# Optimization experiments

Measured on AMD Instinct MI355X. Metric: run time of the kernel, lower is better.

Reference implementation:

```python
import jax, jax.numpy as jnp
import numpy as np

N = 6144
F_IN, H1, H2, EMB = 512, 256, 128, 64
ALPHA = 0.2  # LeakyReLU negative slope
NEG_INF = -9e15


def setup_inputs() -> dict:
    key = jax.random.key(0)
    ks = jax.random.split(key, 12)
    x = jax.random.normal(ks[0], (N, F_IN), dtype=jnp.float32)
    adj = (jax.random.uniform(ks[1], (N, N)) < 0.01).astype(jnp.float32)
    adj = jnp.maximum(adj, jnp.eye(N, dtype=jnp.float32))
    M = jax.random.uniform(ks[2], (N, N), dtype=jnp.float32)

    def glorot(k, shape):
        lim = float(np.sqrt(6.0 / (shape[0] + shape[1])))
        return jax.random.uniform(k, shape, jnp.float32, -lim, lim)

    params = {
        "W1": glorot(ks[3], (F_IN, H1)), "a_s1": glorot(ks[4], (H1, 1)), "a_n1": glorot(ks[5], (H1, 1)),
        "W2": glorot(ks[6], (H1, H2)),  "a_s2": glorot(ks[7], (H2, 1)), "a_n2": glorot(ks[8], (H2, 1)),
        "W3": glorot(ks[9], (H2, EMB)), "a_s3": glorot(ks[10], (EMB, 1)), "a_n3": glorot(ks[11], (EMB, 1)),
    }
    return {"x": x, "adj": adj, "M": M, **params}


def _gat_layer(x, adj, M, W, a_s, a_n):
    h = x @ W                                   # [N, d_out]
    e = (h @ a_s) + (h @ a_n).T                 # [N, N] pairwise logits
    e = jax.nn.leaky_relu(e * M, ALPHA)
    e = jnp.where(adj > 0, e, NEG_INF)
    att = jax.nn.softmax(e, axis=1)             # masked row softmax
    return jax.nn.elu(att @ h)


def reference(x, adj, M, W1, a_s1, a_n1, W2, a_s2, a_n2, W3, a_s3, a_n3):
    h = _gat_layer(x, adj, M, W1, a_s1, a_n1)
    h = _gat_layer(h, adj, M, W2, a_s2, a_n2)
    h = _gat_layer(h, adj, M, W3, a_s3, a_n3)
    z = h / jnp.maximum(jnp.linalg.norm(h, axis=1, keepdims=True), 1e-12)
    A_pred = jax.nn.sigmoid(z @ z.T)
    return (A_pred, z)
```

## Files before the change

### kernel.cpp

```cpp
#include <hip/hip_runtime.h>
#include <hip/hip_bf16.h>
#include <math.h>

#define NROW 6144
#define LRELU_ALPHA 0.2f
#define MAXD 128

typedef __attribute__((ext_vector_type(8))) __bf16 bf16x8;
typedef __attribute__((ext_vector_type(16))) float f32x16;

__global__ __launch_bounds__(256) void prep_small(
    const float* __restrict__ W1, const float* __restrict__ W2, const float* __restrict__ W3,
    __bf16* __restrict__ w1h, __bf16* __restrict__ w1l,
    __bf16* __restrict__ w2h, __bf16* __restrict__ w2l,
    __bf16* __restrict__ w3h, __bf16* __restrict__ w3l,
    const float* __restrict__ as1, const float* __restrict__ an1,
    const float* __restrict__ as2, const float* __restrict__ an2,
    const float* __restrict__ as3, const float* __restrict__ an3,
    float* __restrict__ wsa1, float* __restrict__ wna1,
    float* __restrict__ wsa2, float* __restrict__ wna2,
    float* __restrict__ wsa3, float* __restrict__ wna3) {
  int b = blockIdx.x;
  if (b < 672) {
    int idx = b * 256 + threadIdx.x;
    const float* W; __bf16 *wh, *wl; int K, D;
    if (idx < 131072) { W = W1; wh = w1h; wl = w1l; K = 512; D = 256; }
    else if (idx < 163840) { idx -= 131072; W = W2; wh = w2h; wl = w2l; K = 256; D = 128; }
    else { idx -= 163840; if (idx >= 8192) return; W = W3; wh = w3h; wl = w3l; K = 128; D = 64; }
    int k = idx / D, d = idx - k * D;
    float v = W[idx];
    __bf16 h = (__bf16)v;
    wh[(size_t)d * K + k] = h;
    wl[(size_t)d * K + k] = (__bf16)(v - (float)h);
    return;
  }
  int t = (b - 672) * 256 + threadIdx.x;
  if (t < 512) {
    float s = 0.f, n = 0.f;
    for (int d = 0; d < 256; ++d) { float w = W1[t * 256 + d]; s = fmaf(w, as1[d], s); n = fmaf(w, an1[d], n); }
    wsa1[t] = s; wna1[t] = n;
  } else if (t < 768) {
    int k = t - 512;
    float s = 0.f, n = 0.f;
    for (int d = 0; d < 128; ++d) { float w = W2[k * 128 + d]; s = fmaf(w, as2[d], s); n = fmaf(w, an2[d], n); }
    wsa2[k] = s; wna2[k] = n;
  } else if (t < 896) {
    int k = t - 768;
    float s = 0.f, n = 0.f;
    for (int d = 0; d < 64; ++d) { float w = W3[k * 64 + d]; s = fmaf(w, as3[d], s); n = fmaf(w, an3[d], n); }
    wsa3[k] = s; wna3[k] = n;
  }
}

__global__ __launch_bounds__(256) void build_csr(const float* __restrict__ adj,
                                                 const float* __restrict__ Mm,
                                                 int* __restrict__ cnt,
                                                 int* __restrict__ cidx,
                                                 float* __restrict__ cmval) {
  const int row = blockIdx.x;
  const int wv = threadIdx.x >> 6, lane = threadIdx.x & 63;
  __shared__ int wtot[4];
  __shared__ int jsh[MAXD];
  const float4* arow = (const float4*)(adj + (size_t)row * NROW);
  uint32_t mask = 0;
#pragma unroll
  for (int it = 0; it < 6; ++it) {
    float4 a = arow[wv * 384 + it * 64 + lane];
    uint32_t q = (a.x > 0.f ? 1u : 0u) | (a.y > 0.f ? 2u : 0u) |
                 (a.z > 0.f ? 4u : 0u) | (a.w > 0.f ? 8u : 0u);
    mask |= q << (it * 4);
  }
  const int pc = __popc(mask);
  int pre = pc;
#pragma unroll
  for (int off = 1; off < 64; off <<= 1) {
    int t = __shfl_up(pre, off);
    if (lane >= off) pre += t;
  }
  if (lane == 63) wtot[wv] = pre;
  __syncthreads();
  int base = pre - pc;
  for (int w = 0; w < wv; ++w) base += wtot[w];
  const int total = min(wtot[0] + wtot[1] + wtot[2] + wtot[3], MAXD);
  uint32_t m = mask;
  int p = base;
  const int cbase = wv * 1536 + lane * 4;
  while (m) {
    int b = __ffs(m) - 1;
    m &= m - 1;
    if (p < MAXD) jsh[p] = cbase + ((b >> 2) << 8) + (b & 3);
    ++p;
  }
  __syncthreads();
  const float* mrow = Mm + (size_t)row * NROW;
  for (int k = threadIdx.x; k < total; k += 256) {
    int j = jsh[k];
    cidx[(size_t)row * MAXD + k] = j;
    cmval[(size_t)row * MAXD + k] = mrow[j];
  }
  if (threadIdx.x == 0) cnt[row] = total;
}

__global__ __launch_bounds__(256) void gemm_mfma(const float* __restrict__ A,
                                                 const __bf16* __restrict__ Bth,
                                                 const __bf16* __restrict__ Btl,
                                                 const float* __restrict__ wsa,
                                                 const float* __restrict__ wna,
                                                 float* __restrict__ sv,
                                                 float* __restrict__ nv,
                                                 float* __restrict__ C,
                                                 __bf16* __restrict__ Cb, int K, int D) {
  const int wv = threadIdx.x >> 6, lane = threadIdx.x & 63;
  const int l31 = lane & 31, lh = lane >> 5;
  const int ib = blockIdx.x * 64 + (wv >> 1) * 32;
  const int jb = blockIdx.y * 64 + (wv & 1) * 32;
  const float* Arow = A + (size_t)(ib + l31) * K + lh * 8;
  const __bf16* Bh = Bth + (size_t)(jb + l31) * K + lh * 8;
  const __bf16* Bl = Btl + (size_t)(jb + l31) * K + lh * 8;
  const bool do_sn = (blockIdx.y == 0) && ((wv & 1) == 0);
  f32x16 acc;
#pragma unroll
  for (int r = 0; r < 16; ++r) acc[r] = 0.f;
  float ss = 0.f, nn = 0.f;
  for (int k = 0; k < K; k += 16) {
    float4 a0 = *(const float4*)(Arow + k);
    float4 a1 = *(const float4*)(Arow + k + 4);
    bf16x8 bh = *(const bf16x8*)(Bh + k);
    bf16x8 bl = *(const bf16x8*)(Bl + k);
    float av[8] = {a0.x, a0.y, a0.z, a0.w, a1.x, a1.y, a1.z, a1.w};
    if (do_sn) {
      float4 s0 = *(const float4*)(wsa + k + lh * 8);
      float4 s1 = *(const float4*)(wsa + k + lh * 8 + 4);
      float4 n0 = *(const float4*)(wna + k + lh * 8);
      float4 n1 = *(const float4*)(wna + k + lh * 8 + 4);
      ss = fmaf(av[0], s0.x, ss); ss = fmaf(av[1], s0.y, ss);
      ss = fmaf(av[2], s0.z, ss); ss = fmaf(av[3], s0.w, ss);
      ss = fmaf(av[4], s1.x, ss); ss = fmaf(av[5], s1.y, ss);
      ss = fmaf(av[6], s1.z, ss); ss = fmaf(av[7], s1.w, ss);
      nn = fmaf(av[0], n0.x, nn); nn = fmaf(av[1], n0.y, nn);
      nn = fmaf(av[2], n0.z, nn); nn = fmaf(av[3], n0.w, nn);
      nn = fmaf(av[4], n1.x, nn); nn = fmaf(av[5], n1.y, nn);
      nn = fmaf(av[6], n1.z, nn); nn = fmaf(av[7], n1.w, nn);
    }
    bf16x8 ah, al;
#pragma unroll
    for (int t = 0; t < 8; ++t) {
      __bf16 h = (__bf16)av[t];
      ah[t] = h;
      al[t] = (__bf16)(av[t] - (float)h);
    }
    acc = __builtin_amdgcn_mfma_f32_32x32x16_bf16(ah, bh, acc, 0, 0, 0);
    acc = __builtin_amdgcn_mfma_f32_32x32x16_bf16(ah, bl, acc, 0, 0, 0);
    acc = __builtin_amdgcn_mfma_f32_32x32x16_bf16(al, bh, acc, 0, 0, 0);
  }
  if (do_sn) {
    ss += __shfl_xor(ss, 32);
    nn += __shfl_xor(nn, 32);
    if (lh == 0) { sv[ib + l31] = ss; nv[ib + l31] = nn; }
  }
#pragma unroll
  for (int r = 0; r < 16; ++r) {
    int rowi = (r & 3) + 8 * (r >> 2) + 4 * lh;
    if (C)  C[(size_t)(ib + rowi) * D + jb + l31] = acc[r];
    if (Cb) Cb[(size_t)(ib + rowi) * D + jb + l31] = (__bf16)acc[r];
  }
}

template <int D, int WPR, bool BF16G, bool NORM>
__global__ __launch_bounds__(256) void attn_csr(const float* __restrict__ h,
                                                const __bf16* __restrict__ hb,
                                                const int* __restrict__ cnt,
                                                const int* __restrict__ cidx,
                                                const float* __restrict__ cmval,
                                                const float* __restrict__ sv,
                                                const float* __restrict__ nv,
                                                float* __restrict__ out,
                                                __bf16* __restrict__ zb) {
  constexpr int RPB = 4 / WPR;
  constexpr int CW = D / WPR;
  constexpr int NQ = BF16G ? 2 : CW / 64;
  __shared__ float ws[4][MAXD];
  __shared__ int js[4][MAXD];
  const int wv = threadIdx.x >> 6, lane = threadIdx.x & 63;
  const int row = blockIdx.x * RPB + wv / WPR;
  const int half = wv % WPR;
  const int c = cnt[row];
  const float si = sv[row];
  const size_t cb = (size_t)row * MAXD;

  float e0 = -1e30f, e1 = -1e30f;
  int j0 = 0, j1 = 0;
  if (lane < c) {
    j0 = cidx[cb + lane];
    float v = (si + nv[j0]) * cmval[cb + lane];
    e0 = v > 0.f ? v : LRELU_ALPHA * v;
  }
  if (lane + 64 < c) {
    j1 = cidx[cb + lane + 64];
    float v = (si + nv[j1]) * cmval[cb + lane + 64];
    e1 = v > 0.f ? v : LRELU_ALPHA * v;
  }
  float mx = fmaxf(e0, e1);
#pragma unroll
  for (int off = 32; off; off >>= 1) mx = fmaxf(mx, __shfl_xor(mx, off));
  float w0 = lane < c ? __expf(e0 - mx) : 0.f;
  float w1 = lane + 64 < c ? __expf(e1 - mx) : 0.f;
  float s = w0 + w1;
#pragma unroll
  for (int off = 32; off; off >>= 1) s += __shfl_xor(s, off);
  const float inv = 1.f / s;
  ws[wv][lane] = w0 * inv;
  ws[wv][lane + 64] = w1 * inv;
  js[wv][lane] = j0;
  js[wv][lane + 64] = j1;
  const int cbase = half * CW;
  float acc[NQ];
#pragma unroll
  for (int q = 0; q < NQ; ++q) acc[q] = 0.f;
  if (BF16G) {
#pragma unroll 8
    for (int k = 0; k < c; ++k) {
      const float wk = ws[wv][k];
      const uint32_t* hr = (const uint32_t*)(hb + (size_t)js[wv][k] * D + cbase);
      uint32_t v = hr[lane];
      acc[0] = fmaf(wk, __uint_as_float(v << 16), acc[0]);
      acc[1] = fmaf(wk, __uint_as_float(v & 0xffff0000u), acc[1]);
    }
    float2 o;
    o.x = acc[0] > 0.f ? acc[0] : expm1f(acc[0]);
    o.y = acc[1] > 0.f ? acc[1] : expm1f(acc[1]);
    *(float2*)(out + (size_t)row * D + cbase + lane * 2) = o;
  } else {
#pragma unroll 8
    for (int k = 0; k < c; ++k) {
      const float wk = ws[wv][k];
      const float* hr = h + (size_t)js[wv][k] * D + cbase;
#pragma unroll
      for (int q = 0; q < NQ; ++q) acc[q] = fmaf(wk, hr[lane + q * 64], acc[q]);
    }
    if (!NORM) {
#pragma unroll
      for (int q = 0; q < NQ; ++q) {
        float a = acc[q];
        out[(size_t)row * D + cbase + lane + q * 64] = a > 0.f ? a : expm1f(a);
      }
    } else {
      float a = acc[0];
      a = a > 0.f ? a : expm1f(a);
      float sq = a * a;
#pragma unroll
      for (int off = 32; off; off >>= 1) sq += __shfl_xor(sq, off);
      float zv = a / fmaxf(sqrtf(sq), 1e-12f);
      out[(size_t)row * 64 + lane] = zv;
      zb[(size_t)row * 64 + lane] = (__bf16)zv;
    }
  }
}

__global__ __launch_bounds__(256) void decoder_mfma(const __bf16* __restrict__ zb,
                                                    float* __restrict__ out) {
  const int wv = threadIdx.x >> 6, lane = threadIdx.x & 63;
  const int ib = blockIdx.y * 64 + (wv >> 1) * 32;
  const int jb = blockIdx.x * 64 + (wv & 1) * 32;
  const int l31 = lane & 31, lh = lane >> 5;
  const __bf16* Arow = zb + (size_t)(ib + l31) * 64 + lh * 8;
  const __bf16* Brow = zb + (size_t)(jb + l31) * 64 + lh * 8;
  f32x16 acc;
#pragma unroll
  for (int r = 0; r < 16; ++r) acc[r] = 0.f;
#pragma unroll
  for (int kk = 0; kk < 4; ++kk) {
    bf16x8 af = *(const bf16x8*)(Arow + kk * 16);
    bf16x8 bfv = *(const bf16x8*)(Brow + kk * 16);
    acc = __builtin_amdgcn_mfma_f32_32x32x16_bf16(af, bfv, acc, 0, 0, 0);
  }
#pragma unroll
  for (int r = 0; r < 16; ++r) {
    int rowi = (r & 3) + 8 * (r >> 2) + 4 * lh;
    float v = 1.f / (1.f + __expf(-acc[r]));
    out[(size_t)(ib + rowi) * NROW + jb + l31] = v;
  }
}

extern "C" void kernel_launch(void* const* d_in, const int* in_sizes, int n_in,
                              void* d_out, int out_size, void* d_ws, size_t ws_size,
                              hipStream_t stream) {
  const float* x   = (const float*)d_in[0];
  const float* adj = (const float*)d_in[1];
  const float* Mm  = (const float*)d_in[2];
  const float* W1  = (const float*)d_in[3];
  const float* as1 = (const float*)d_in[4];
  const float* an1 = (const float*)d_in[5];
  const float* W2  = (const float*)d_in[6];
  const float* as2 = (const float*)d_in[7];
  const float* an2 = (const float*)d_in[8];
  const float* W3  = (const float*)d_in[9];
  const float* as3 = (const float*)d_in[10];
  const float* an3 = (const float*)d_in[11];

  float* out = (float*)d_out;
  float* z = out + (size_t)NROW * NROW;

  float* ws = (float*)d_ws;
  float* hA   = ws;
  float* hB   = hA + (size_t)NROW * 256;
  float* sv   = hB + (size_t)NROW * 256;
  float* nv   = sv + NROW;
  float* cmv  = nv + NROW;
  int*   cix  = (int*)(cmv + (size_t)NROW * MAXD);
  int*   cct  = cix + (size_t)NROW * MAXD;
  __bf16* zb  = (__bf16*)(cct + NROW);
  __bf16* w1h = zb + (size_t)NROW * 64;
  __bf16* w1l = w1h + 512 * 256;
  __bf16* w2h = w1l + 512 * 256;
  __bf16* w2l = w2h + 256 * 128;
  __bf16* w3h = w2l + 256 * 128;
  __bf16* w3l = w3h + 128 * 64;
  float* wsa1 = (float*)(w3l + 128 * 64);
  float* wna1 = wsa1 + 512;
  float* wsa2 = wna1 + 512;
  float* wna2 = wsa2 + 256;
  float* wsa3 = wna2 + 256;
  float* wna3 = wsa3 + 128;
  __bf16* hAb = (__bf16*)(wna3 + 128);

  dim3 b256(256);

  prep_small<<<dim3(676), b256, 0, stream>>>(
      W1, W2, W3, w1h, w1l, w2h, w2l, w3h, w3l,
      as1, an1, as2, an2, as3, an3, wsa1, wna1, wsa2, wna2, wsa3, wna3);

  build_csr<<<dim3(NROW), b256, 0, stream>>>(adj, Mm, cct, cix, cmv);

  gemm_mfma<<<dim3(NROW / 64, 4), b256, 0, stream>>>(x, w1h, w1l, wsa1, wna1, sv, nv, nullptr, hAb, 512, 256);
  attn_csr<256, 2, true, false><<<dim3(NROW / 2), b256, 0, stream>>>(nullptr, hAb, cct, cix, cmv, sv, nv, hB, nullptr);

  gemm_mfma<<<dim3(NROW / 64, 2), b256, 0, stream>>>(hB, w2h, w2l, wsa2, wna2, sv, nv, nullptr, hAb, 256, 128);
  attn_csr<128, 1, true, false><<<dim3(NROW / 4), b256, 0, stream>>>(nullptr, hAb, cct, cix, cmv, sv, nv, hB, nullptr);

  gemm_mfma<<<dim3(NROW / 64, 1), b256, 0, stream>>>(hB, w3h, w3l, wsa3, wna3, sv, nv, hA, nullptr, 128, 64);
  attn_csr<64, 1, false, true><<<dim3(NROW / 4), b256, 0, stream>>>(hA, nullptr, cct, cix, cmv, sv, nv, z, zb);

  decoder_mfma<<<dim3(NROW / 64, NROW / 64), b256, 0, stream>>>(zb, out);
}
```

Baseline: 196.8 us.

## Fuse GAT layers and decoder into one cooperative persistent kernel

Merges the CSR build and the weight prep into a single launch. All GEMM, attention and decoder stages now run in one cooperative persistent kernel, with grid-wide syncs between stages and grid-stride loops over the old block indices. This removes per-kernel launch overhead and the gaps between the many small stages. In exchange the grid size is capped by occupancy (up to 8 blocks per CU over 256 CUs). The grid syncs and the shared-memory and register use of the fused kernel may lower occupancy for the heavy decoder stage.

```diff
diff --git a/kernel.cpp b/kernel.cpp
--- a/kernel.cpp
+++ b/kernel.cpp
@@ -1,6 +1,9 @@
 #include <hip/hip_runtime.h>
 #include <hip/hip_bf16.h>
+#include <hip/hip_cooperative_groups.h>
 #include <math.h>
+
+namespace cg = cooperative_groups;
 
 #define NROW 6144
 #define LRELU_ALPHA 0.2f
@@ -9,7 +12,9 @@
 typedef __attribute__((ext_vector_type(8))) __bf16 bf16x8;
 typedef __attribute__((ext_vector_type(16))) float f32x16;
 
-__global__ __launch_bounds__(256) void prep_small(
+__global__ __launch_bounds__(256) void prep_csr(
+    const float* __restrict__ adj, const float* __restrict__ Mm,
+    int* __restrict__ cnt, int* __restrict__ cidx, float* __restrict__ cmval,
     const float* __restrict__ W1, const float* __restrict__ W2, const float* __restrict__ W3,
     __bf16* __restrict__ w1h, __bf16* __restrict__ w1l,
     __bf16* __restrict__ w2h, __bf16* __restrict__ w2l,
@@ -21,6 +26,52 @@
     float* __restrict__ wsa2, float* __restrict__ wna2,
     float* __restrict__ wsa3, float* __restrict__ wna3) {
   int b = blockIdx.x;
+  if (b < NROW) {
+    const int row = b;
+    const int wv = threadIdx.x >> 6, lane = threadIdx.x & 63;
+    __shared__ int wtot[4];
+    __shared__ int jsh[MAXD];
+    const float4* arow = (const float4*)(adj + (size_t)row * NROW);
+    uint32_t mask = 0;
+#pragma unroll
+    for (int it = 0; it < 6; ++it) {
+      float4 a = arow[wv * 384 + it * 64 + lane];
+      uint32_t q = (a.x > 0.f ? 1u : 0u) | (a.y > 0.f ? 2u : 0u) |
+                   (a.z > 0.f ? 4u : 0u) | (a.w > 0.f ? 8u : 0u);
+      mask |= q << (it * 4);
+    }
+    const int pc = __popc(mask);
+    int pre = pc;
+#pragma unroll
+    for (int off = 1; off < 64; off <<= 1) {
+      int t = __shfl_up(pre, off);
+      if (lane >= off) pre += t;
+    }
+    if (lane == 63) wtot[wv] = pre;
+    __syncthreads();
+    int base = pre - pc;
+    for (int w = 0; w < wv; ++w) base += wtot[w];
+    const int total = min(wtot[0] + wtot[1] + wtot[2] + wtot[3], MAXD);
+    uint32_t m = mask;
+    int p = base;
+    const int cbase = wv * 1536 + lane * 4;
+    while (m) {
+      int bit = __ffs(m) - 1;
+      m &= m - 1;
+      if (p < MAXD) jsh[p] = cbase + ((bit >> 2) << 8) + (bit & 3);
+      ++p;
+    }
+    __syncthreads();
+    const float* mrow = Mm + (size_t)row * NROW;
+    for (int k = threadIdx.x; k < total; k += 256) {
+      int j = jsh[k];
+      cidx[(size_t)row * MAXD + k] = j;
+      cmval[(size_t)row * MAXD + k] = mrow[j];
+    }
+    if (threadIdx.x == 0) cnt[row] = total;
+    return;
+  }
+  b -= NROW;
   if (b < 672) {
     int idx = b * 256 + threadIdx.x;
     const float* W; __bf16 *wh, *wl; int K, D;
@@ -52,72 +103,24 @@
   }
 }
 
-__global__ __launch_bounds__(256) void build_csr(const float* __restrict__ adj,
-                                                 const float* __restrict__ Mm,
-                                                 int* __restrict__ cnt,
-                                                 int* __restrict__ cidx,
-                                                 float* __restrict__ cmval) {
-  const int row = blockIdx.x;
-  const int wv = threadIdx.x >> 6, lane = threadIdx.x & 63;
-  __shared__ int wtot[4];
-  __shared__ int jsh[MAXD];
-  const float4* arow = (const float4*)(adj + (size_t)row * NROW);
-  uint32_t mask = 0;
-#pragma unroll
-  for (int it = 0; it < 6; ++it) {
-    float4 a = arow[wv * 384 + it * 64 + lane];
-    uint32_t q = (a.x > 0.f ? 1u : 0u) | (a.y > 0.f ? 2u : 0u) |
-                 (a.z > 0.f ? 4u : 0u) | (a.w > 0.f ? 8u : 0u);
-    mask |= q << (it * 4);
-  }
-  const int pc = __popc(mask);
-  int pre = pc;
-#pragma unroll
-  for (int off = 1; off < 64; off <<= 1) {
-    int t = __shfl_up(pre, off);
-    if (lane >= off) pre += t;
-  }
-  if (lane == 63) wtot[wv] = pre;
-  __syncthreads();
-  int base = pre - pc;
-  for (int w = 0; w < wv; ++w) base += wtot[w];
-  const int total = min(wtot[0] + wtot[1] + wtot[2] + wtot[3], MAXD);
-  uint32_t m = mask;
-  int p = base;
-  const int cbase = wv * 1536 + lane * 4;
-  while (m) {
-    int b = __ffs(m) - 1;
-    m &= m - 1;
-    if (p < MAXD) jsh[p] = cbase + ((b >> 2) << 8) + (b & 3);
-    ++p;
-  }
-  __syncthreads();
-  const float* mrow = Mm + (size_t)row * NROW;
-  for (int k = threadIdx.x; k < total; k += 256) {
-    int j = jsh[k];
-    cidx[(size_t)row * MAXD + k] = j;
-    cmval[(size_t)row * MAXD + k] = mrow[j];
-  }
-  if (threadIdx.x == 0) cnt[row] = total;
-}
-
-__global__ __launch_bounds__(256) void gemm_mfma(const float* __restrict__ A,
-                                                 const __bf16* __restrict__ Bth,
-                                                 const __bf16* __restrict__ Btl,
-                                                 const float* __restrict__ wsa,
-                                                 const float* __restrict__ wna,
-                                                 float* __restrict__ sv,
-                                                 float* __restrict__ nv,
-                                                 float* __restrict__ C,
-                                                 __bf16* __restrict__ Cb, int K, int D) {
+__device__ __forceinline__ void gemm_body(int bx, int by,
+                                          const float* __restrict__ A,
+                                          const __bf16* __restrict__ Bth,
+                                          const __bf16* __restrict__ Btl,
+                                          const float* __restrict__ wsa,
+                                          const float* __restrict__ wna,
+                                          float* __restrict__ sv,
+                                          float* __restrict__ nv,
+                                          float* __restrict__ C,
+                                          __bf16* __restrict__ Cb, int K, int D) {
   const int wv = threadIdx.x >> 6, lane = threadIdx.x & 63;
   const int l31 = lane & 31, lh = lane >> 5;
-  const int ib = blockIdx.x * 64 + (wv >> 1) * 32;
-  const int jb = blockIdx.y * 64 + (wv & 1) * 32;
+  const int ib = bx * 64 + (wv >> 1) * 32;
+  const int jb = by * 64 + (wv & 1) * 32;
   const float* Arow = A + (size_t)(ib + l31) * K + lh * 8;
   const __bf16* Bh = Bth + (size_t)(jb + l31) * K + lh * 8;
   const __bf16* Bl = Btl + (size_t)(jb + l31) * K + lh * 8;
-  const bool do_sn = (blockIdx.y == 0) && ((wv & 1) == 0);
+  const bool do_sn = (by == 0) && ((wv & 1) == 0);
   f32x16 acc;
 #pragma unroll
   for (int r = 0; r < 16; ++r) acc[r] = 0.f;
@@ -167,22 +170,22 @@
 }
 
 template <int D, int WPR, bool BF16G, bool NORM>
-__global__ __launch_bounds__(256) void attn_csr(const float* __restrict__ h,
-                                                const __bf16* __restrict__ hb,
-                                                const int* __restrict__ cnt,
-                                                const int* __restrict__ cidx,
-                                                const float* __restrict__ cmval,
-                                                const float* __restrict__ sv,
-                                                const float* __restrict__ nv,
-                                                float* __restrict__ out,
-                                                __bf16* __restrict__ zb) {
+__device__ __forceinline__ void attn_body(int blk,
+                                          const float* __restrict__ h,
+                                          const __bf16* __restrict__ hb,
+                                          const int* __restrict__ cnt,
+                                          const int* __restrict__ cidx,
+                                          const float* __restrict__ cmval,
+                                          const float* __restrict__ sv,
+                                          const float* __restrict__ nv,
+                                          float* __restrict__ out,
+                                          __bf16* __restrict__ zbp,
+                                          float (*ws)[MAXD], int (*js)[MAXD]) {
   constexpr int RPB = 4 / WPR;
   constexpr int CW = D / WPR;
   constexpr int NQ = BF16G ? 2 : CW / 64;
-  __shared__ float ws[4][MAXD];
-  __shared__ int js[4][MAXD];
   const int wv = threadIdx.x >> 6, lane = threadIdx.x & 63;
-  const int row = blockIdx.x * RPB + wv / WPR;
+  const int row = blk * RPB + wv / WPR;
   const int half = wv % WPR;
   const int c = cnt[row];
   const float si = sv[row];
@@ -252,16 +255,17 @@
       for (int off = 32; off; off >>= 1) sq += __shfl_xor(sq, off);
       float zv = a / fmaxf(sqrtf(sq), 1e-12f);
       out[(size_t)row * 64 + lane] = zv;
-      zb[(size_t)row * 64 + lane] = (__bf16)zv;
-    }
-  }
-}
-
-__global__ __launch_bounds__(256) void decoder_mfma(const __bf16* __restrict__ zb,
-                                                    float* __restrict__ out) {
+      zbp[(size_t)row * 64 + lane] = (__bf16)zv;
+    }
+  }
+}
+
+__device__ __forceinline__ void decoder_body(int bj, int bi,
+                                             const __bf16* __restrict__ zb,
+                                             float* __restrict__ out) {
   const int wv = threadIdx.x >> 6, lane = threadIdx.x & 63;
-  const int ib = blockIdx.y * 64 + (wv >> 1) * 32;
-  const int jb = blockIdx.x * 64 + (wv & 1) * 32;
+  const int ib = bi * 64 + (wv >> 1) * 32;
+  const int jb = bj * 64 + (wv & 1) * 32;
   const int l31 = lane & 31, lh = lane >> 5;
   const __bf16* Arow = zb + (size_t)(ib + l31) * 64 + lh * 8;
   const __bf16* Brow = zb + (size_t)(jb + l31) * 64 + lh * 8;
@@ -280,6 +284,48 @@
     float v = 1.f / (1.f + __expf(-acc[r]));
     out[(size_t)(ib + rowi) * NROW + jb + l31] = v;
   }
+}
+
+__global__ __launch_bounds__(256) void gat_all(
+    const float* __restrict__ x,
+    const __bf16* __restrict__ w1h, const __bf16* __restrict__ w1l,
+    const __bf16* __restrict__ w2h, const __bf16* __restrict__ w2l,
+    const __bf16* __restrict__ w3h, const __bf16* __restrict__ w3l,
+    const float* __restrict__ wsa1, const float* __restrict__ wna1,
+    const float* __restrict__ wsa2, const float* __restrict__ wna2,
+    const float* __restrict__ wsa3, const float* __restrict__ wna3,
+    const int* __restrict__ cct, const int* __restrict__ cix,
+    const float* __restrict__ cmv,
+    float* __restrict__ sv, float* __restrict__ nv,
+    float* __restrict__ hA, float* __restrict__ hB,
+    __bf16* __restrict__ hAb,
+    float* __restrict__ z, __bf16* __restrict__ zb,
+    float* __restrict__ out) {
+  cg::grid_group grid = cg::this_grid();
+  const int G = gridDim.x;
+  __shared__ float sws[4][MAXD];
+  __shared__ int sjs[4][MAXD];
+
+  for (int j = blockIdx.x; j < 384; j += G)
+    gemm_body(j >> 2, j & 3, x, w1h, w1l, wsa1, wna1, sv, nv, nullptr, hAb, 512, 256);
+  grid.sync();
+  for (int j = blockIdx.x; j < 3072; j += G)
+    attn_body<256, 2, true, false>(j, nullptr, hAb, cct, cix, cmv, sv, nv, hB, nullptr, sws, sjs);
+  grid.sync();
+  for (int j = blockIdx.x; j < 192; j += G)
+    gemm_body(j >> 1, j & 1, hB, w2h, w2l, wsa2, wna2, sv, nv, nullptr, hAb, 256, 128);
+  grid.sync();
+  for (int j = blockIdx.x; j < 1536; j += G)
+    attn_body<128, 1, true, false>(j, nullptr, hAb, cct, cix, cmv, sv, nv, hB, nullptr, sws, sjs);
+  grid.sync();
+  for (int j = blockIdx.x; j < 96; j += G)
+    gemm_body(j, 0, hB, w3h, w3l, wsa3, wna3, sv, nv, hA, nullptr, 128, 64);
+  grid.sync();
+  for (int j = blockIdx.x; j < 1536; j += G)
+    attn_body<64, 1, false, true>(j, hA, nullptr, cct, cix, cmv, sv, nv, z, zb, sws, sjs);
+  grid.sync();
+  for (int j = blockIdx.x; j < 9216; j += G)
+    decoder_body(j % 96, j / 96, zb, out);
 }
 
 extern "C" void kernel_launch(void* const* d_in, const int* in_sizes, int n_in,
@@ -301,8 +347,8 @@
   float* out = (float*)d_out;
   float* z = out + (size_t)NROW * NROW;
 
-  float* ws = (float*)d_ws;
-  float* hA   = ws;
+  float* wsp = (float*)d_ws;
+  float* hA   = wsp;
   float* hB   = hA + (size_t)NROW * 256;
   float* sv   = hB + (size_t)NROW * 256;
   float* nv   = sv + NROW;
@@ -326,20 +372,23 @@
 
   dim3 b256(256);
 
-  prep_small<<<dim3(676), b256, 0, stream>>>(
-      W1, W2, W3, w1h, w1l, w2h, w2l, w3h, w3l,
+  prep_csr<<<dim3(NROW + 676), b256, 0, stream>>>(
+      adj, Mm, cct, cix, cmv, W1, W2, W3, w1h, w1l, w2h, w2l, w3h, w3l,
       as1, an1, as2, an2, as3, an3, wsa1, wna1, wsa2, wna2, wsa3, wna3);
 
-  build_csr<<<dim3(NROW), b256, 0, stream>>>(adj, Mm, cct, cix, cmv);
-
-  gemm_mfma<<<dim3(NROW / 64, 4), b256, 0, stream>>>(x, w1h, w1l, wsa1, wna1, sv, nv, nullptr, hAb, 512, 256);
-  attn_csr<256, 2, true, false><<<dim3(NROW / 2), b256, 0, stream>>>(nullptr, hAb, cct, cix, cmv, sv, nv, hB, nullptr);
-
-  gemm_mfma<<<dim3(NROW / 64, 2), b256, 0, stream>>>(hB, w2h, w2l, wsa2, wna2, sv, nv, nullptr, hAb, 256, 128);
-  attn_csr<128, 1, true, false><<<dim3(NROW / 4), b256, 0, stream>>>(nullptr, hAb, cct, cix, cmv, sv, nv, hB, nullptr);
-
-  gemm_mfma<<<dim3(NROW / 64, 1), b256, 0, stream>>>(hB, w3h, w3l, wsa3, wna3, sv, nv, hA, nullptr, 128, 64);
-  attn_csr<64, 1, false, true><<<dim3(NROW / 4), b256, 0, stream>>>(hA, nullptr, cct, cix, cmv, sv, nv, z, zb);
-
-  decoder_mfma<<<dim3(NROW / 64, NROW / 64), b256, 0, stream>>>(zb, out);
-}
+  int nb = 0;
+  (void)hipOccupancyMaxActiveBlocksPerMultiprocessor(&nb, gat_all, 256, 0);
+  if (nb < 1) nb = 1;
+  if (nb > 8) nb = 8;
+  int G = nb * 256;
+
+  void* args[] = {(void*)&x,
+                  (void*)&w1h, (void*)&w1l, (void*)&w2h, (void*)&w2l,
+                  (void*)&w3h, (void*)&w3l,
+                  (void*)&wsa1, (void*)&wna1, (void*)&wsa2, (void*)&wna2,
+                  (void*)&wsa3, (void*)&wna3,
+                  (void*)&cct, (void*)&cix, (void*)&cmv,
+                  (void*)&sv, (void*)&nv, (void*)&hA, (void*)&hB, (void*)&hAb,
+                  (void*)&z, (void*)&zb, (void*)&out};
+  (void)hipLaunchCooperativeKernel(gat_all, dim3(G), b256, args, 0, stream);
+}
```

After: 575.2 us. +192.2%, slower.
